# Optimization experiments

Measured on AMD Instinct MI355X. Metric: run time of the kernel, lower is better.

## Reference

```python
import jax, jax.numpy as jnp
from jax import lax
import numpy as np

B, F, T, D, H = 16, 20, 128, 300, 256

def _lstm_scan(x, mask, W, U, b):
    # x: [N, T, D], mask: [N, T] bool. Keras gate order: i, f, g(c), o.
    N = x.shape[0]
    xz = jnp.einsum('ntd,dh->nth', x, W) + b  # [N, T, 4H] input projection, hoisted out of scan
    def step(carry, inp):
        h, c = carry
        z_x, m = inp
        z = z_x + h @ U
        i, f, g, o = jnp.split(z, 4, axis=-1)
        c_new = jax.nn.sigmoid(f) * c + jax.nn.sigmoid(i) * jnp.tanh(g)
        h_new = jax.nn.sigmoid(o) * jnp.tanh(c_new)
        m = m[:, None]
        # Keras masking: masked steps copy previous state/output through
        h = jnp.where(m, h_new, h)
        c = jnp.where(m, c_new, c)
        return (h, c), h
    init = (jnp.zeros((N, H), x.dtype), jnp.zeros((N, H), x.dtype))
    _, hs = lax.scan(step, init, (jnp.swapaxes(xz, 0, 1), jnp.swapaxes(mask, 0, 1)))
    return jnp.swapaxes(hs, 0, 1)  # [N, T, H]

def setup_inputs() -> dict:
    key = jax.random.key(0)
    ks = jax.random.split(key, 8)
    facts = jax.random.normal(ks[0], (B, F, T, D), dtype=jnp.float32)
    lengths = jax.random.randint(ks[1], (B, F), T // 2, T + 1)
    mask = jnp.arange(T)[None, None, :] < lengths[..., None]  # valid-prefix padding mask [B,F,T]
    s_in = 1.0 / np.sqrt(D)
    s_h = 1.0 / np.sqrt(H)
    W_fwd = jax.random.normal(ks[2], (D, 4 * H), dtype=jnp.float32) * s_in
    U_fwd = jax.random.normal(ks[3], (H, 4 * H), dtype=jnp.float32) * s_h
    b_fwd = jnp.zeros((4 * H,), dtype=jnp.float32).at[H:2 * H].set(1.0)  # unit forget bias
    W_bwd = jax.random.normal(ks[4], (D, 4 * H), dtype=jnp.float32) * s_in
    U_bwd = jax.random.normal(ks[5], (H, 4 * H), dtype=jnp.float32) * s_h
    b_bwd = jnp.zeros((4 * H,), dtype=jnp.float32).at[H:2 * H].set(1.0)
    return {"facts": facts, "mask": mask, "W_fwd": W_fwd, "U_fwd": U_fwd, "b_fwd": b_fwd,
            "W_bwd": W_bwd, "U_bwd": U_bwd, "b_bwd": b_bwd}

def reference(facts, mask, W_fwd, U_fwd, b_fwd, W_bwd, U_bwd, b_bwd):
    # Flatten (B, F) -> N sequences, as in FactEncoder.call
    x = facts.reshape(B * F, T, D)
    m = mask.reshape(B * F, T)
    h_f = _lstm_scan(x, m, W_fwd, U_fwd, b_fwd)
    # Bidirectional backward branch: reverse time, run, reverse output back
    h_b = _lstm_scan(x[:, ::-1], m[:, ::-1], W_bwd, U_bwd, b_bwd)[:, ::-1]
    out = jnp.concatenate([h_f, h_b], axis=-1)  # merge_mode='concat'
    return out.reshape(B, F, T, 2 * H)
```

## Files before the change

### kernel.cpp

```cpp
#include <hip/hip_runtime.h>
#include <hip/hip_bf16.h>

constexpr int Bc   = 16;
constexpr int Fc   = 20;
constexpr int T    = 128;
constexpr int D    = 300;
constexpr int H    = 256;
constexpr int NSEQ = Bc * Fc;
constexpr int G4   = 4 * H;
constexpr int DP   = 320;

constexpr int WTN = 2 * G4 * DP;
constexpr int UTN = 2 * G4 * H;

typedef __attribute__((ext_vector_type(8))) short  short8_t;
typedef __attribute__((ext_vector_type(4))) float  f32x4;

__device__ __forceinline__ short8_t ld8(const short* p) { return *(const short8_t*)p; }
__device__ __forceinline__ f32x4 mf(short8_t a, short8_t b, f32x4 c) {
    return __builtin_amdgcn_mfma_f32_16x16x32_bf16(a, b, c, 0, 0, 0);
}
__device__ __forceinline__ float b2f(short s) {
    unsigned u = ((unsigned)(unsigned short)s) << 16;
    return __builtin_bit_cast(float, u);
}
__device__ __forceinline__ short f2b(float f) {
    unsigned u = __builtin_bit_cast(unsigned, f);
    u += 0x7fffu + ((u >> 16) & 1u);
    return (short)(u >> 16);
}
__device__ __forceinline__ float blo(unsigned w) { return __builtin_bit_cast(float, w << 16); }
__device__ __forceinline__ float bhi(unsigned w) { return __builtin_bit_cast(float, w & 0xffff0000u); }
__device__ __forceinline__ float sigf(float x) {
    float e = __builtin_amdgcn_exp2f(x * -1.44269504f);
    return __builtin_amdgcn_rcpf(1.0f + e);
}
__device__ __forceinline__ float tanhf_(float x) {
    float e = __builtin_amdgcn_exp2f(x * -2.88539008f);
    return __builtin_amdgcn_rcpf(1.0f + e) * 2.0f - 1.0f;
}
__device__ __forceinline__ bool in_is_fp32(const unsigned* bfw) {
    return bfw[256] == 0x3F800000u;
}
__device__ __forceinline__ float in_val(const void* p, long long i, bool is32) {
    return is32 ? ((const float*)p)[i] : b2f(((const short*)p)[i]);
}

__global__ void prep_wu(const void* __restrict__ Wf, const void* __restrict__ Uf,
                        const void* __restrict__ Wb, const void* __restrict__ Ub,
                        const unsigned* __restrict__ bfw,
                        short* __restrict__ wt, short* __restrict__ ut)
{
    const bool is32 = in_is_fp32(bfw);
    int idx = blockIdx.x * 256 + threadIdx.x;
    if (idx < WTN) {
        int d_ = idx / (G4 * DP), j = idx - d_ * (G4 * DP);
        int n  = j / DP, k = j - n * DP;
        const void* W = d_ ? Wb : Wf;
        wt[idx] = (k < D) ? f2b(in_val(W, (long long)k * G4 + n, is32)) : (short)0;
    } else if (idx < WTN + UTN) {
        int i  = idx - WTN;
        int d_ = i / (G4 * H), j = i - d_ * (G4 * H);
        int n  = j / H, k = j - n * H;
        const void* U = d_ ? Ub : Uf;
        int kp = (k & ~31) | ((k & 15) << 1) | ((k >> 4) & 1);
        ut[i - k + kp] = f2b(in_val(U, (long long)k * G4 + n, is32));
    }
}

__global__ void prep_xp(const void* __restrict__ facts, const unsigned* __restrict__ bfw,
                        short* __restrict__ xpc, int Tc, int t00, int t01)
{
    const bool is32 = in_is_fp32(bfw);
    long long total = 2LL * NSEQ * Tc * DP;
    long long idx = (long long)blockIdx.x * 256 + threadIdx.x;
    if (idx >= total) return;
    int perdir = NSEQ * Tc * DP;
    int d_  = (int)(idx / perdir);
    int rem = (int)(idx - (long long)d_ * perdir);
    int seq = rem / (Tc * DP);
    int r2  = rem - seq * (Tc * DP);
    int tl  = r2 / DP;
    int k   = r2 - tl * DP;
    int t0  = d_ ? t01 : t00;
    long long frow = (long long)(seq * T + t0 + tl) * D;
    xpc[idx] = (k < D) ? f2b(in_val(facts, frow + k, is32)) : (short)0;
}

__global__ void gemm_xz(const short* __restrict__ xpc, const short* __restrict__ wt,
                        const void* __restrict__ bfv, const void* __restrict__ bbv,
                        const unsigned* __restrict__ bfw,
                        short* __restrict__ xzc, int Tc)
{
    const bool is32 = in_is_fp32(bfw);
    const int dir = blockIdx.z;
    const short* wtd  = wt + (size_t)dir * G4 * DP;
    const void*  bias = dir ? bbv : bfv;
    const short* xpA = xpc + (size_t)dir * NSEQ * Tc * DP + (size_t)blockIdx.y * 128 * DP;
    short* xzd = xzc + (size_t)dir * NSEQ * Tc * G4;

    const int m0 = blockIdx.y * 128;
    const int n0 = blockIdx.x * 128;
    const int tid = threadIdx.x;
    const int wid = tid >> 6, lane = tid & 63, quad = lane >> 4, l15 = lane & 15;
    const int wm = wid >> 1, wn = wid & 1;

    __shared__ __align__(16) short Al[128 * 40];
    __shared__ __align__(16) short Bl[128 * 40];

    const short* wtB = wtd + (size_t)n0 * DP;

    f32x4 acc[4][4];
#pragma unroll
    for (int mi = 0; mi < 4; ++mi)
#pragma unroll
        for (int ni = 0; ni < 4; ++ni) acc[mi][ni] = (f32x4){0.f, 0.f, 0.f, 0.f};

    for (int kk = 0; kk < 10; ++kk) {
#pragma unroll
        for (int i = 0; i < 2; ++i) {
            int cid = tid + i * 256;
            int row = cid >> 2, cc = cid & 3;
            *(short8_t*)&Al[row * 40 + cc * 8] = ld8(xpA + (size_t)row * DP + kk * 32 + cc * 8);
            *(short8_t*)&Bl[row * 40 + cc * 8] = ld8(wtB + (size_t)row * DP + kk * 32 + cc * 8);
        }
        __syncthreads();
        short8_t a[4], b[4];
#pragma unroll
        for (int mi = 0; mi < 4; ++mi)
            a[mi] = ld8(&Al[(wm * 64 + mi * 16 + l15) * 40 + quad * 8]);
#pragma unroll
        for (int ni = 0; ni < 4; ++ni)
            b[ni] = ld8(&Bl[(wn * 64 + ni * 16 + l15) * 40 + quad * 8]);
#pragma unroll
        for (int mi = 0; mi < 4; ++mi)
#pragma unroll
            for (int ni = 0; ni < 4; ++ni)
                acc[mi][ni] = mf(a[mi], b[ni], acc[mi][ni]);
        __syncthreads();
    }

#pragma unroll
    for (int ni = 0; ni < 4; ++ni) {
        int col = n0 + wn * 64 + ni * 16 + l15;
        float bv = is32 ? ((const float*)bias)[col] : b2f(((const short*)bias)[col]);
        int pos = (col & ~31) | ((col & 15) << 1) | ((col >> 4) & 1);
#pragma unroll
        for (int mi = 0; mi < 4; ++mi) {
            int row = m0 + wm * 64 + mi * 16 + quad * 4;
#pragma unroll
            for (int r = 0; r < 4; ++r)
                xzd[(size_t)(row + r) * G4 + pos] = f2b(acc[mi][ni][r] + bv);
        }
    }
}

__global__ __launch_bounds__(512, 2)
void lstm_chunk(const short* __restrict__ xzc, const short* __restrict__ utp,
                const void* __restrict__ maskp, void* __restrict__ out,
                const unsigned* __restrict__ bfw,
                short* __restrict__ h_ws, float* __restrict__ c_ws,
                int Tc, int cbase, int first)
{
    const bool is32 = in_is_fp32(bfw);
    const int tid = threadIdx.x;
    const int wv = tid >> 6, lane = tid & 63, quad = lane >> 4, l15 = lane & 15;
    const int g = blockIdx.x;
    const int dir = g / 20, s0 = (g % 20) * 16;

    const short* ut  = utp + (size_t)dir * G4 * H;
    const short* xzd = xzc + (size_t)dir * NSEQ * Tc * G4;

    constexpr int HR = 296;
    __shared__ __align__(16) short hbuf[2][16 * HR];
    __shared__ __align__(16) short ulds[8 * 2 * 8 * 64 * 8];
    __shared__ unsigned char mbuf[16 * 128];

    {
        const unsigned* mw = (const unsigned*)maskp;
        unsigned w0 = mw[0];
        int mode = (w0 == 1u || w0 == 0x3F800000u) ? 0 : (w0 == 0x3F803F80u ? 1 : 2);
        for (int i = tid; i < 16 * 128; i += 512) {
            int r = i >> 7, t = i & 127;
            int gi = (s0 + r) * T + t;
            unsigned char mv;
            if (mode == 0)      mv = (mw[gi] != 0) ? 1 : 0;
            else if (mode == 1) mv = (((const unsigned short*)maskp)[gi] != 0) ? 1 : 0;
            else                mv = ((const unsigned char*)maskp)[gi];
            mbuf[i] = mv;
        }
    }

    const int fb = l15 * H + quad * 8;
    const int c7 = (3 * 256 + 32 * wv + 16) * H + fb;

    short8_t ureg[5][8];
    {
        const int cr[5] = { (0*256 + 32*wv +  0) * H + fb,
                            (0*256 + 32*wv + 16) * H + fb,
                            (1*256 + 32*wv +  0) * H + fb,
                            (1*256 + 32*wv + 16) * H + fb,
                            (2*256 + 32*wv +  0) * H + fb };
#pragma unroll
        for (int a = 0; a < 5; ++a)
#pragma unroll
            for (int kk = 0; kk < 8; ++kk)
                ureg[a][kk] = ld8(ut + cr[a] + kk * 32);
    }
#pragma unroll
    for (int a = 0; a < 5; ++a)
#pragma unroll
        for (int kk = 0; kk < 8; ++kk)
            asm volatile("" : "+v"(ureg[a][kk]));

    {
        const int c5 = (2 * 256 + 32 * wv + 16) * H + fb;
        const int c6 = (3 * 256 + 32 * wv +  0) * H + fb;
#pragma unroll
        for (int kk = 0; kk < 8; ++kk) {
            *(short8_t*)&ulds[(((wv * 2 + 0) * 8 + kk) * 64 + lane) * 8] = ld8(ut + c5 + kk * 32);
            *(short8_t*)&ulds[(((wv * 2 + 1) * 8 + kk) * 64 + lane) * 8] = ld8(ut + c6 + kk * 32);
        }
    }

    for (int i = tid; i < 16 * 256; i += 512) {
        int sq = i >> 8, d = i & 255;
        int pos = (d & ~31) | ((d & 15) << 1) | ((d >> 4) & 1);
        hbuf[0][sq * HR + pos] = first ? (short)0
            : h_ws[(size_t)(dir * NSEQ + s0 + sq) * H + d];
    }
    float cst[2][4], hst[2][4];
#pragma unroll
    for (int jj = 0; jj < 2; ++jj)
#pragma unroll
        for (int r = 0; r < 4; ++r) {
            size_t sidx = (size_t)(dir * NSEQ + s0 + quad * 4 + r) * H + 32 * wv + 16 * jj + l15;
            hst[jj][r] = first ? 0.f : b2f(h_ws[sidx]);
            cst[jj][r] = first ? 0.f : c_ws[sidx];
        }

    const int dstep = dir ? -1 : 1;
    const int tl0 = dir ? (Tc - 1) : 0;
    const int tg0 = dir ? (T - 1 - cbase) : cbase;

    const unsigned* xzu = (const unsigned*)xzd;
    const int seqb = s0 + quad * 4;
    int xzo0 = (seqb * Tc + tl0) * 512 + 16 * wv + l15;
    int ob0  = (seqb * T + tg0) * (2 * H) + dir * H + 32 * wv + l15;

    short8_t u7[4];
#pragma unroll
    for (int i = 0; i < 4; ++i) u7[i] = ld8(ut + c7 + i * 32);

    __syncthreads();

    int p = 0;
    for (int s = 0; s < Tc; ++s) {
        const int t = dir ? (T - 1 - cbase - s) : (cbase + s);

        f32x4 acc[8];
#pragma unroll
        for (int a = 0; a < 8; ++a) acc[a] = (f32x4){0.f, 0.f, 0.f, 0.f};
        unsigned xzv[4][4];

        const short* hb = &hbuf[p][0];
        __builtin_amdgcn_s_setprio(1);
#pragma unroll
        for (int kk = 0; kk < 8; ++kk) {
            short8_t af = ld8(&hb[l15 * HR + kk * 32 + quad * 8]);
#pragma unroll
            for (int a = 0; a < 5; ++a) acc[a] = mf(af, ureg[a][kk], acc[a]);
            short8_t u5 = ld8(&ulds[(((wv * 2 + 0) * 8 + kk) * 64 + lane) * 8]);
            acc[5] = mf(af, u5, acc[5]);
            short8_t u6 = ld8(&ulds[(((wv * 2 + 1) * 8 + kk) * 64 + lane) * 8]);
            acc[6] = mf(af, u6, acc[6]);
            acc[7] = mf(af, u7[kk & 3], acc[7]);
            u7[kk & 3] = ld8(ut + c7 + (((kk + 4) & 7) * 32));
            if (kk == 2) {
#pragma unroll
                for (int gi = 0; gi < 4; ++gi)
#pragma unroll
                    for (int r = 0; r < 4; ++r)
                        xzv[gi][r] = xzu[xzo0 + r * (Tc * 512) + gi * 128];
            }
        }
        __builtin_amdgcn_s_setprio(0);

#pragma unroll
        for (int r = 0; r < 4; ++r) {
            bool m = mbuf[(quad * 4 + r) * T + t] != 0;
#pragma unroll
            for (int jj = 0; jj < 2; ++jj) {
                float xi = jj ? bhi(xzv[0][r]) : blo(xzv[0][r]);
                float xf = jj ? bhi(xzv[1][r]) : blo(xzv[1][r]);
                float xg = jj ? bhi(xzv[2][r]) : blo(xzv[2][r]);
                float xo = jj ? bhi(xzv[3][r]) : blo(xzv[3][r]);
                float zi = acc[0 + jj][r] + xi;
                float zf = acc[2 + jj][r] + xf;
                float zg = acc[4 + jj][r] + xg;
                float zo = acc[6 + jj][r] + xo;
                float iv = sigf(zi), fv = sigf(zf), gv = tanhf_(zg), ov = sigf(zo);
                float cn = fv * cst[jj][r] + iv * gv;
                float hn = ov * tanhf_(cn);
                cst[jj][r] = m ? cn : cst[jj][r];
                hst[jj][r] = m ? hn : hst[jj][r];
            }
            unsigned hw = (unsigned)(unsigned short)f2b(hst[0][r])
                        | ((unsigned)(unsigned short)f2b(hst[1][r]) << 16);
            *(unsigned*)&hbuf[p ^ 1][(quad * 4 + r) * HR + 32 * wv + 2 * l15] = hw;
            int ob = ob0 + r * (T * 2 * H);
            if (is32) {
                ((float*)out)[ob]      = hst[0][r];
                ((float*)out)[ob + 16] = hst[1][r];
            } else {
                ((short*)out)[ob]      = (short)(hw & 0xffffu);
                ((short*)out)[ob + 16] = (short)(hw >> 16);
            }
        }
        xzo0 += dstep * 512;
        ob0  += dstep * 512;
        p ^= 1;
        asm volatile("s_waitcnt lgkmcnt(0)" ::: "memory");
        __builtin_amdgcn_s_barrier();
        __builtin_amdgcn_sched_barrier(0);
    }

#pragma unroll
    for (int jj = 0; jj < 2; ++jj)
#pragma unroll
        for (int r = 0; r < 4; ++r) {
            size_t sidx = (size_t)(dir * NSEQ + s0 + quad * 4 + r) * H + 32 * wv + 16 * jj + l15;
            h_ws[sidx] = f2b(hst[jj][r]);
            c_ws[sidx] = cst[jj][r];
        }
}

extern "C" void kernel_launch(void* const* d_in, const int* in_sizes, int n_in,
                              void* d_out, int out_size, void* d_ws, size_t ws_size,
                              hipStream_t stream)
{
    const void* facts = d_in[0];
    const void* maskp = d_in[1];
    const void* Wf = d_in[2];
    const void* Uf = d_in[3];
    const void* bf = d_in[4];
    const void* Wb = d_in[5];
    const void* Ub = d_in[6];
    const void* bb = d_in[7];
    const unsigned* bfw = (const unsigned*)bf;

    const unsigned long long fixedB =
        (unsigned long long)(WTN + UTN) * 2 + (2ull * NSEQ * H) * 2 + (2ull * NSEQ * H) * 4 + 1024;
    int Tc = 128;
    while (Tc > 4 && (1720320ull * Tc + fixedB) > ws_size) Tc >>= 1;
    const int nC = T / Tc;

    short* ws   = (short*)d_ws;
    short* xzc  = ws;
    short* xpc  = xzc + (size_t)2 * NSEQ * Tc * G4;
    short* wt   = xpc + (size_t)2 * NSEQ * Tc * DP;
    short* ut   = wt + WTN;
    short* h_ws = ut + UTN;
    float* c_ws = (float*)(h_ws + (size_t)2 * NSEQ * H);

    prep_wu<<<(WTN + UTN + 255) / 256, 256, 0, stream>>>(Wf, Uf, Wb, Ub, bfw, wt, ut);

    const long long xpTotal = 2LL * NSEQ * Tc * DP;
    for (int c = 0; c < nC; ++c) {
        int t00 = c * Tc;
        int t01 = T - (c + 1) * Tc;
        prep_xp<<<(int)((xpTotal + 255) / 256), 256, 0, stream>>>(facts, bfw, xpc, Tc, t00, t01);
        gemm_xz<<<dim3(8, NSEQ * Tc / 128, 2), 256, 0, stream>>>(xpc, wt, bf, bb, bfw, xzc, Tc);
        lstm_chunk<<<40, 512, 0, stream>>>(xzc, ut, maskp, d_out, bfw, h_ws, c_ws,
                                           Tc, c * Tc, c == 0 ? 1 : 0);
    }
}
```

Before: 837.6 us.

## Replace per-step block barrier with per-wave LDS flags and staggered k-order

Removes the workgroup-wide s_barrier at the end of each recurrence step. Each wave now publishes a step counter in LDS once its h-slice is written. In the next step, each wave starts its k-loop on its own slice and spin-waits only on the flag of the wave that produced each later slice. The register and global U-weight fragments are re-indexed to match this rotated k order. The aim is to let waves overlap instead of all stalling at one barrier, at the cost of LDS polling and reliance on volatile LDS ordering.

```diff
diff --git a/kernel.cpp b/kernel.cpp
--- a/kernel.cpp
+++ b/kernel.cpp
@@ -175,6 +175,9 @@
     __shared__ __align__(16) short hbuf[2][16 * HR];
     __shared__ __align__(16) short ulds[8 * 2 * 8 * 64 * 8];
     __shared__ unsigned char mbuf[16 * 128];
+    __shared__ int flg[8 * 16];
+
+    if (tid < 8) flg[tid * 16] = -1;
 
     {
         const unsigned* mw = (const unsigned*)maskp;
@@ -204,14 +207,14 @@
 #pragma unroll
         for (int a = 0; a < 5; ++a)
 #pragma unroll
-            for (int kk = 0; kk < 8; ++kk)
-                ureg[a][kk] = ld8(ut + cr[a] + kk * 32);
+            for (int j = 0; j < 8; ++j)
+                ureg[a][j] = ld8(ut + cr[a] + (((wv + j) & 7) * 32));
     }
 #pragma unroll
     for (int a = 0; a < 5; ++a)
 #pragma unroll
-        for (int kk = 0; kk < 8; ++kk)
-            asm volatile("" : "+v"(ureg[a][kk]));
+        for (int j = 0; j < 8; ++j)
+            asm volatile("" : "+v"(ureg[a][j]));
 
     {
         const int c5 = (2 * 256 + 32 * wv + 16) * H + fb;
@@ -250,7 +253,7 @@
 
     short8_t u7[4];
 #pragma unroll
-    for (int i = 0; i < 4; ++i) u7[i] = ld8(ut + c7 + i * 32);
+    for (int i = 0; i < 4; ++i) u7[i] = ld8(ut + c7 + (((wv + i) & 7) * 32));
 
     __syncthreads();
 
@@ -266,17 +269,23 @@
         const short* hb = &hbuf[p][0];
         __builtin_amdgcn_s_setprio(1);
 #pragma unroll
-        for (int kk = 0; kk < 8; ++kk) {
+        for (int j = 0; j < 8; ++j) {
+            const int kk = (wv + j) & 7;
+            if (j > 0) {
+                volatile int* fp = &flg[kk * 16];
+                while (*fp < s - 1) { }
+                asm volatile("" ::: "memory");
+            }
             short8_t af = ld8(&hb[l15 * HR + kk * 32 + quad * 8]);
 #pragma unroll
-            for (int a = 0; a < 5; ++a) acc[a] = mf(af, ureg[a][kk], acc[a]);
+            for (int a = 0; a < 5; ++a) acc[a] = mf(af, ureg[a][j], acc[a]);
             short8_t u5 = ld8(&ulds[(((wv * 2 + 0) * 8 + kk) * 64 + lane) * 8]);
             acc[5] = mf(af, u5, acc[5]);
             short8_t u6 = ld8(&ulds[(((wv * 2 + 1) * 8 + kk) * 64 + lane) * 8]);
             acc[6] = mf(af, u6, acc[6]);
-            acc[7] = mf(af, u7[kk & 3], acc[7]);
-            u7[kk & 3] = ld8(ut + c7 + (((kk + 4) & 7) * 32));
-            if (kk == 2) {
+            acc[7] = mf(af, u7[j & 3], acc[7]);
+            u7[j & 3] = ld8(ut + c7 + (((kk + 4) & 7) * 32));
+            if (j == 2) {
 #pragma unroll
                 for (int gi = 0; gi < 4; ++gi)
 #pragma unroll
@@ -317,12 +326,12 @@
                 ((short*)out)[ob + 16] = (short)(hw >> 16);
             }
         }
+        asm volatile("s_waitcnt lgkmcnt(0)" ::: "memory");
+        if (lane == 0) *(volatile int*)&flg[wv * 16] = s;
+
         xzo0 += dstep * 512;
         ob0  += dstep * 512;
         p ^= 1;
-        asm volatile("s_waitcnt lgkmcnt(0)" ::: "memory");
-        __builtin_amdgcn_s_barrier();
-        __builtin_amdgcn_sched_barrier(0);
     }
 
 #pragma unroll
```

New measurement: 1.258 ms. 1.5x slower.
